# Optimization experiments

Measured on AMD Instinct MI355X. Metric: run time of the kernel, lower is better.

Reference implementation:

```python
import jax, jax.numpy as jnp
import numpy as np
from jax import lax

B, C_IN, C_OUT, H, W, K, PAD = 4, 64, 64, 96, 96, 3, 1
K2 = K * K


def setup_inputs() -> dict:
    key = jax.random.key(0)
    k1, k2, k3, k4, k5 = jax.random.split(key, 5)
    x = jax.random.normal(k1, (B, C_IN, H, W), jnp.float32)
    offset = jax.random.normal(k2, (B, 2 * K2, H, W), jnp.float32)
    weight = jax.random.normal(k3, (C_OUT, C_IN, K, K), jnp.float32) * 0.05
    mask_weight = jax.random.normal(k4, (K2, C_IN, K, K), jnp.float32) * 0.05
    mask_bias = jax.random.normal(k5, (K2,), jnp.float32) * 0.05
    return {"x": x, "offset": offset, "weight": weight,
            "mask_weight": mask_weight, "mask_bias": mask_bias}


def _deform_conv2d(x, offset, weight, mask):
    # torchvision ordering: per kernel tap k, offset[:, 2k] is dy, offset[:, 2k+1] is dx
    off_y = offset[:, 0::2]  # [B, K2, H, W]
    off_x = offset[:, 1::2]
    ky, kx = jnp.meshgrid(jnp.arange(K), jnp.arange(K), indexing="ij")
    ky = ky.reshape(K2).astype(x.dtype)
    kx = kx.reshape(K2).astype(x.dtype)
    hh = jnp.arange(H, dtype=x.dtype)
    ww = jnp.arange(W, dtype=x.dtype)
    base_y = hh[None, :, None] - PAD + ky[:, None, None]   # [K2, H, 1]
    base_x = ww[None, None, :] - PAD + kx[:, None, None]   # [K2, 1, W]
    py = base_y[None] + off_y                               # [B, K2, H, W]
    px = base_x[None] + off_x

    y0 = jnp.floor(py)
    x0 = jnp.floor(px)
    wy = py - y0   # bilinear weights
    wx = px - x0
    y0i = y0.astype(jnp.int32)
    x0i = x0.astype(jnp.int32)

    x_flat = x.reshape(B, C_IN, H * W)

    def gather(yy, xx):
        valid = (yy >= 0) & (yy < H) & (xx >= 0) & (xx < W)
        idx = jnp.clip(yy, 0, H - 1) * W + jnp.clip(xx, 0, W - 1)  # [B,K2,H,W]
        idx_f = idx.reshape(B, -1)
        v = jax.vmap(lambda xf, i: xf[:, i])(x_flat, idx_f)  # [B, C, K2*H*W]
        v = v.reshape(B, C_IN, K2, H, W)
        return v * valid[:, None].astype(v.dtype)

    v00 = gather(y0i, x0i)
    v01 = gather(y0i, x0i + 1)
    v10 = gather(y0i + 1, x0i)
    v11 = gather(y0i + 1, x0i + 1)

    wy_ = wy[:, None]  # [B,1,K2,H,W]
    wx_ = wx[:, None]
    sampled = (v00 * (1 - wy_) * (1 - wx_) + v01 * (1 - wy_) * wx_
               + v10 * wy_ * (1 - wx_) + v11 * wy_ * wx_)
    sampled = sampled * mask[:, None]  # modulate by sigmoid mask

    w2 = weight.reshape(C_OUT, C_IN, K2)
    return jnp.einsum("bckhw,ock->bohw", sampled, w2)


def reference(x, offset, weight, mask_weight, mask_bias):
    mask_logits = lax.conv_general_dilated(
        x, mask_weight, window_strides=(1, 1), padding=[(PAD, PAD), (PAD, PAD)],
        dimension_numbers=("NCHW", "OIHW", "NCHW"))
    mask = jax.nn.sigmoid(mask_logits + mask_bias[None, :, None, None])
    return _deform_conv2d(x, offset, weight, mask)
```

## Files before the change

### kernel.cpp

```cpp
#include <hip/hip_runtime.h>
#include <math.h>

#define BB 4
#define CI 64
#define CO 64
#define HH 96
#define WW 96
#define HW (HH*WW)
#define K2 9
#define NT (HW/64)
#define PADC 1

typedef __attribute__((ext_vector_type(8))) short short8;
typedef __attribute__((ext_vector_type(4))) float float4v;

#define XT_USHORTS ((size_t)BB*HW*64)
#define WF_USHORTS (18*64*32)
#define MWF_USHORTS (18*16*32)

__device__ __forceinline__ float bf2f(short s) {
    return __uint_as_float(((unsigned int)(unsigned short)s) << 16);
}
__device__ __forceinline__ short f2bf(float f) {
    unsigned int u = __float_as_uint(f);
    u = (u + 0x7fffu + ((u >> 16) & 1u)) >> 16;
    return (short)u;
}

__device__ __forceinline__ void unswz(int bid, int* b, int* tile) {
    int g = bid & 7, r = bid >> 3;
    *b = g & 3;
    *tile = (g >> 2) * 72 + r;
}

__global__ __launch_bounds__(256) void xt_kernel(const float* __restrict__ x,
                                                 unsigned short* __restrict__ xT) {
    __shared__ unsigned short ts[64][72];
    int t = threadIdx.x;
    int b, tl; unswz(blockIdx.x, &b, &tl);
    int p0 = tl * 64;
    const float* xb = x + (size_t)b * CI * HW + p0;
    int pq = t & 15, cg = t >> 4;
    #pragma unroll
    for (int i = 0; i < 4; i++) {
        int c = cg + i * 16;
        float4v v = *(const float4v*)(xb + (size_t)c * HW + pq * 4);
        ts[pq * 4 + 0][c] = (unsigned short)f2bf(v[0]);
        ts[pq * 4 + 1][c] = (unsigned short)f2bf(v[1]);
        ts[pq * 4 + 2][c] = (unsigned short)f2bf(v[2]);
        ts[pq * 4 + 3][c] = (unsigned short)f2bf(v[3]);
    }
    __syncthreads();
    int px = t >> 2, cq = t & 3;
    unsigned short* xo = xT + ((size_t)b * HW + p0 + px) * 64 + cq * 16;
    short8 v0 = *(const short8*)&ts[px][cq * 16];
    short8 v1 = *(const short8*)&ts[px][cq * 16 + 8];
    *(short8*)xo = v0;
    *(short8*)(xo + 8) = v1;
}

__global__ __launch_bounds__(256) void pack_kernel(const float* __restrict__ wgt,
                                                   const float* __restrict__ mw,
                                                   unsigned short* __restrict__ Wf,
                                                   unsigned short* __restrict__ MWf) {
    int i = blockIdx.x * 256 + threadIdx.x;
    if (i < WF_USHORTS) {
        int frag = i >> 11;
        int o = (i >> 5) & 63;
        int tt = i & 31;
        int k = frag >> 1, cc = frag & 1;
        int c = cc * 32 + tt;
        Wf[i] = (unsigned short)f2bf(wgt[o * 576 + c * 9 + k]);
    } else if (i < WF_USHORTS + MWF_USHORTS) {
        int e = i - WF_USHORTS;
        int frag = e >> 9;
        int m = (e >> 5) & 15;
        int tt = e & 31;
        int q = frag >> 1, cc = frag & 1;
        int c = cc * 32 + tt;
        MWf[e] = (m < 9) ? (unsigned short)f2bf(mw[m * 576 + c * 9 + q]) : 0;
    }
}

__global__ __launch_bounds__(256) void fused_kernel(const float* __restrict__ off,
                                                    const float* __restrict__ mbias,
                                                    const unsigned short* __restrict__ xT,
                                                    const unsigned short* __restrict__ Wf,
                                                    const unsigned short* __restrict__ MWf,
                                                    float* __restrict__ out) {
    __shared__ float s_mask[K2][64];
    __shared__ int   s_idx[K2][4][64];
    __shared__ float s_w[K2][4][64];

    int t = threadIdx.x;
    int lane = t & 63, wv = t >> 6;
    int n = lane & 15, quad = lane >> 4;
    int b, tl; unswz(blockIdx.x, &b, &tl);
    int p0 = tl * 64;
    int pxl = wv * 16 + n;
    int p = p0 + pxl;
    int h = p / WW, wc = p % WW;
    const unsigned short* xTb = xT + (size_t)b * HW * 64;

    {
        float4v acc = {0.f, 0.f, 0.f, 0.f};
        #pragma unroll
        for (int q = 0; q < 9; q++) {
            int hh = h + q / 3 - 1, ww2 = wc + q % 3 - 1;
            bool valid = (hh >= 0) && (hh < HH) && (ww2 >= 0) && (ww2 < WW);
            int nidx = valid ? (hh * WW + ww2) : 0;
            const unsigned short* src = xTb + (size_t)nidx * 64 + quad * 8;
            #pragma unroll
            for (int cc = 0; cc < 2; cc++) {
                short8 bfrag = {0, 0, 0, 0, 0, 0, 0, 0};
                if (valid) bfrag = *(const short8*)(src + cc * 32);
                short8 afrag = *(const short8*)(MWf + ((size_t)((q * 2 + cc) * 16 + n)) * 32 + quad * 8);
                acc = __builtin_amdgcn_mfma_f32_16x16x32_bf16(afrag, bfrag, acc, 0, 0, 0);
            }
        }
        #pragma unroll
        for (int r = 0; r < 4; r++) {
            int row = quad * 4 + r;
            if (row < 9) {
                float s = acc[r] + mbias[row];
                s_mask[row][pxl] = 1.f / (1.f + expf(-s));
            }
        }
    }
    __syncthreads();

    for (int e = t; e < K2 * 64; e += 256) {
        int k = e >> 6, pe = e & 63;
        int pp = p0 + pe;
        int hh0 = pp / WW, ww0 = pp % WW;
        int ky = k / 3, kx = k % 3;
        float oy = off[((size_t)b * 2 * K2 + 2 * k) * HW + pp];
        float ox = off[((size_t)b * 2 * K2 + 2 * k + 1) * HW + pp];
        float m = s_mask[k][pe];
        float py = (float)(hh0 - PADC + ky) + oy;
        float pxf = (float)(ww0 - PADC + kx) + ox;
        float y0f = floorf(py), x0f = floorf(pxf);
        float wy = py - y0f, wx = pxf - x0f;
        int y0 = (int)y0f, x0 = (int)x0f;
        int y1 = y0 + 1, x1 = x0 + 1;
        int y0c = min(max(y0, 0), HH - 1), y1c = min(max(y1, 0), HH - 1);
        int x0c = min(max(x0, 0), WW - 1), x1c = min(max(x1, 0), WW - 1);
        bool vy0 = (y0 >= 0) && (y0 < HH), vy1 = (y1 >= 0) && (y1 < HH);
        bool vx0 = (x0 >= 0) && (x0 < WW), vx1 = (x1 >= 0) && (x1 < WW);
        float w00 = (1.f - wy) * (1.f - wx) * m; if (!(vy0 && vx0)) w00 = 0.f;
        float w01 = (1.f - wy) * wx * m;         if (!(vy0 && vx1)) w01 = 0.f;
        float w10 = wy * (1.f - wx) * m;         if (!(vy1 && vx0)) w10 = 0.f;
        float w11 = wy * wx * m;                 if (!(vy1 && vx1)) w11 = 0.f;
        s_idx[k][0][pe] = y0c * WW + x0c;
        s_idx[k][1][pe] = y0c * WW + x1c;
        s_idx[k][2][pe] = y1c * WW + x0c;
        s_idx[k][3][pe] = y1c * WW + x1c;
        s_w[k][0][pe] = w00; s_w[k][1][pe] = w01;
        s_w[k][2][pe] = w10; s_w[k][3][pe] = w11;
    }
    __syncthreads();

    float4v acc0 = {0.f, 0.f, 0.f, 0.f};
    float4v acc1 = {0.f, 0.f, 0.f, 0.f};
    float4v acc2 = {0.f, 0.f, 0.f, 0.f};
    float4v acc3 = {0.f, 0.f, 0.f, 0.f};

    const unsigned short* xq = xTb + quad * 8;
    short8 st[2][8];

    auto loadK = [&](int k, short8* dst) {
        int i0 = s_idx[k][0][pxl], i1 = s_idx[k][1][pxl];
        int i2 = s_idx[k][2][pxl], i3 = s_idx[k][3][pxl];
        dst[0] = *(const short8*)(xq + (size_t)i0 * 64);
        dst[1] = *(const short8*)(xq + (size_t)i0 * 64 + 32);
        dst[2] = *(const short8*)(xq + (size_t)i1 * 64);
        dst[3] = *(const short8*)(xq + (size_t)i1 * 64 + 32);
        dst[4] = *(const short8*)(xq + (size_t)i2 * 64);
        dst[5] = *(const short8*)(xq + (size_t)i2 * 64 + 32);
        dst[6] = *(const short8*)(xq + (size_t)i3 * 64);
        dst[7] = *(const short8*)(xq + (size_t)i3 * 64 + 32);
    };

    loadK(0, st[0]);
    loadK(1, st[1]);

    #pragma unroll
    for (int k = 0; k < 9; k++) {
        float w0 = s_w[k][0][pxl], w1 = s_w[k][1][pxl];
        float w2 = s_w[k][2][pxl], w3 = s_w[k][3][pxl];
        short8 cur[8];
        #pragma unroll
        for (int j = 0; j < 8; j++) cur[j] = st[k & 1][j];
        if (k + 2 < 9) loadK(k + 2, st[k & 1]);
        #pragma unroll
        for (int cc = 0; cc < 2; cc++) {
            short8 bfrag;
            #pragma unroll
            for (int j = 0; j < 8; j++) {
                float v = bf2f(cur[cc][j])     * w0 + bf2f(cur[2 + cc][j]) * w1 +
                          bf2f(cur[4 + cc][j]) * w2 + bf2f(cur[6 + cc][j]) * w3;
                bfrag[j] = f2bf(v);
            }
            const unsigned short* wp = Wf + (size_t)((k * 2 + cc) * 64) * 32 + quad * 8;
            short8 a0 = *(const short8*)(wp + (0 * 16 + n) * 32);
            short8 a1 = *(const short8*)(wp + (1 * 16 + n) * 32);
            short8 a2 = *(const short8*)(wp + (2 * 16 + n) * 32);
            short8 a3 = *(const short8*)(wp + (3 * 16 + n) * 32);
            acc0 = __builtin_amdgcn_mfma_f32_16x16x32_bf16(a0, bfrag, acc0, 0, 0, 0);
            acc1 = __builtin_amdgcn_mfma_f32_16x16x32_bf16(a1, bfrag, acc1, 0, 0, 0);
            acc2 = __builtin_amdgcn_mfma_f32_16x16x32_bf16(a2, bfrag, acc2, 0, 0, 0);
            acc3 = __builtin_amdgcn_mfma_f32_16x16x32_bf16(a3, bfrag, acc3, 0, 0, 0);
        }
    }

    float* ob = out + (size_t)b * CO * HW + p0 + pxl;
    #pragma unroll
    for (int r = 0; r < 4; r++) {
        ob[(size_t)(0 * 16 + quad * 4 + r) * HW] = acc0[r];
        ob[(size_t)(1 * 16 + quad * 4 + r) * HW] = acc1[r];
        ob[(size_t)(2 * 16 + quad * 4 + r) * HW] = acc2[r];
        ob[(size_t)(3 * 16 + quad * 4 + r) * HW] = acc3[r];
    }
}

extern "C" void kernel_launch(void* const* d_in, const int* in_sizes, int n_in,
                              void* d_out, int out_size, void* d_ws, size_t ws_size,
                              hipStream_t stream) {
    const float* x   = (const float*)d_in[0];
    const float* off = (const float*)d_in[1];
    const float* wgt = (const float*)d_in[2];
    const float* mw  = (const float*)d_in[3];
    const float* mb  = (const float*)d_in[4];
    float* out = (float*)d_out;

    unsigned short* xT  = (unsigned short*)d_ws;
    unsigned short* Wf  = xT + XT_USHORTS;
    unsigned short* MWf = Wf + WF_USHORTS;

    hipLaunchKernelGGL(xt_kernel, dim3(BB * NT), dim3(256), 0, stream, x, xT);
    hipLaunchKernelGGL(pack_kernel, dim3((WF_USHORTS + MWF_USHORTS + 255) / 256), dim3(256),
                       0, stream, wgt, mw, Wf, MWf);
    hipLaunchKernelGGL(fused_kernel, dim3(BB * NT), dim3(256), 0, stream,
                       off, mb, xT, Wf, MWf, out);
}
```

Baseline: 122.2 us.

## Split input channels across waves with half-size pixel tiles and merge prep kernels

The fused kernel now handles 32 pixels per block and splits the 64 input channels between pairs of waves. Mask logits and output partial sums are reduced through shared memory, and the grid doubles, which raises parallelism and cuts per-thread gather and register load. The transpose and weight-pack kernels are merged into one launch to save launch overhead. In exchange it adds an extra barrier and LDS reduction, and it drops the two-stage software prefetch of gathered values.

```diff
diff --git a/kernel.cpp b/kernel.cpp
--- a/kernel.cpp
+++ b/kernel.cpp
@@ -9,6 +9,8 @@
 #define HW (HH*WW)
 #define K2 9
 #define NT (HW/64)
+#define TPX 32
+#define NTT (HW/TPX)
 #define PADC 1
 
 typedef __attribute__((ext_vector_type(8))) short short8;
@@ -27,58 +29,62 @@
     return (short)u;
 }
 
-__device__ __forceinline__ void unswz(int bid, int* b, int* tile) {
+__device__ __forceinline__ void unswz64(int bid, int* b, int* tile) {
     int g = bid & 7, r = bid >> 3;
     *b = g & 3;
     *tile = (g >> 2) * 72 + r;
 }
-
-__global__ __launch_bounds__(256) void xt_kernel(const float* __restrict__ x,
-                                                 unsigned short* __restrict__ xT) {
+__device__ __forceinline__ void unswz32(int bid, int* b, int* tile) {
+    int g = bid & 7, r = bid >> 3;
+    *b = g & 3;
+    *tile = (g >> 2) * 144 + r;
+}
+
+__global__ __launch_bounds__(256) void prep_kernel(const float* __restrict__ x,
+                                                   const float* __restrict__ wgt,
+                                                   const float* __restrict__ mw,
+                                                   unsigned short* __restrict__ xT,
+                                                   unsigned short* __restrict__ Wf,
+                                                   unsigned short* __restrict__ MWf) {
     __shared__ unsigned short ts[64][72];
     int t = threadIdx.x;
-    int b, tl; unswz(blockIdx.x, &b, &tl);
-    int p0 = tl * 64;
-    const float* xb = x + (size_t)b * CI * HW + p0;
-    int pq = t & 15, cg = t >> 4;
-    #pragma unroll
-    for (int i = 0; i < 4; i++) {
-        int c = cg + i * 16;
-        float4v v = *(const float4v*)(xb + (size_t)c * HW + pq * 4);
-        ts[pq * 4 + 0][c] = (unsigned short)f2bf(v[0]);
-        ts[pq * 4 + 1][c] = (unsigned short)f2bf(v[1]);
-        ts[pq * 4 + 2][c] = (unsigned short)f2bf(v[2]);
-        ts[pq * 4 + 3][c] = (unsigned short)f2bf(v[3]);
-    }
-    __syncthreads();
-    int px = t >> 2, cq = t & 3;
-    unsigned short* xo = xT + ((size_t)b * HW + p0 + px) * 64 + cq * 16;
-    short8 v0 = *(const short8*)&ts[px][cq * 16];
-    short8 v1 = *(const short8*)&ts[px][cq * 16 + 8];
-    *(short8*)xo = v0;
-    *(short8*)(xo + 8) = v1;
-}
-
-__global__ __launch_bounds__(256) void pack_kernel(const float* __restrict__ wgt,
-                                                   const float* __restrict__ mw,
-                                                   unsigned short* __restrict__ Wf,
-                                                   unsigned short* __restrict__ MWf) {
-    int i = blockIdx.x * 256 + threadIdx.x;
-    if (i < WF_USHORTS) {
-        int frag = i >> 11;
-        int o = (i >> 5) & 63;
-        int tt = i & 31;
-        int k = frag >> 1, cc = frag & 1;
-        int c = cc * 32 + tt;
-        Wf[i] = (unsigned short)f2bf(wgt[o * 576 + c * 9 + k]);
-    } else if (i < WF_USHORTS + MWF_USHORTS) {
-        int e = i - WF_USHORTS;
-        int frag = e >> 9;
-        int m = (e >> 5) & 15;
-        int tt = e & 31;
-        int q = frag >> 1, cc = frag & 1;
-        int c = cc * 32 + tt;
-        MWf[e] = (m < 9) ? (unsigned short)f2bf(mw[m * 576 + c * 9 + q]) : 0;
+    if (blockIdx.x < BB * NT) {
+        int b, tl; unswz64(blockIdx.x, &b, &tl);
+        int p0 = tl * 64;
+        const float* xb = x + (size_t)b * CI * HW + p0;
+        int pq = t & 15, cg = t >> 4;
+        #pragma unroll
+        for (int i = 0; i < 4; i++) {
+            int c = cg + i * 16;
+            float4v v = *(const float4v*)(xb + (size_t)c * HW + pq * 4);
+            ts[pq * 4 + 0][c] = (unsigned short)f2bf(v[0]);
+            ts[pq * 4 + 1][c] = (unsigned short)f2bf(v[1]);
+            ts[pq * 4 + 2][c] = (unsigned short)f2bf(v[2]);
+            ts[pq * 4 + 3][c] = (unsigned short)f2bf(v[3]);
+        }
+        __syncthreads();
+        int px = t >> 2, cq = t & 3;
+        unsigned short* xo = xT + ((size_t)b * HW + p0 + px) * 64 + cq * 16;
+        *(short8*)xo       = *(const short8*)&ts[px][cq * 16];
+        *(short8*)(xo + 8) = *(const short8*)&ts[px][cq * 16 + 8];
+    } else {
+        int i = (blockIdx.x - BB * NT) * 256 + t;
+        if (i < WF_USHORTS) {
+            int frag = i >> 11;
+            int o = (i >> 5) & 63;
+            int tt = i & 31;
+            int k = frag >> 1, cc = frag & 1;
+            int c = cc * 32 + tt;
+            Wf[i] = (unsigned short)f2bf(wgt[o * 576 + c * 9 + k]);
+        } else if (i < WF_USHORTS + MWF_USHORTS) {
+            int e = i - WF_USHORTS;
+            int frag = e >> 9;
+            int m = (e >> 5) & 15;
+            int tt = e & 31;
+            int q = frag >> 1, cc = frag & 1;
+            int c = cc * 32 + tt;
+            MWf[e] = (m < 9) ? (unsigned short)f2bf(mw[m * 576 + c * 9 + q]) : 0;
+        }
     }
 }
 
@@ -88,55 +94,52 @@
                                                     const unsigned short* __restrict__ Wf,
                                                     const unsigned short* __restrict__ MWf,
                                                     float* __restrict__ out) {
-    __shared__ float s_mask[K2][64];
-    __shared__ int   s_idx[K2][4][64];
-    __shared__ float s_w[K2][4][64];
+    __shared__ float s_mred[2][K2][TPX];
+    __shared__ int   s_idx[K2][4][TPX];
+    __shared__ float s_w[K2][4][TPX];
+    __shared__ float s_part[2][16][64];
 
     int t = threadIdx.x;
     int lane = t & 63, wv = t >> 6;
+    int pg = wv & 1, ch = wv >> 1;
     int n = lane & 15, quad = lane >> 4;
-    int b, tl; unswz(blockIdx.x, &b, &tl);
-    int p0 = tl * 64;
-    int pxl = wv * 16 + n;
+    int b, tl; unswz32(blockIdx.x, &b, &tl);
+    int p0 = tl * TPX;
+    int pxl = pg * 16 + n;
     int p = p0 + pxl;
     int h = p / WW, wc = p % WW;
     const unsigned short* xTb = xT + (size_t)b * HW * 64;
+    int cbase = ch * 32 + quad * 8;
 
     {
-        float4v acc = {0.f, 0.f, 0.f, 0.f};
+        float4v macc = {0.f, 0.f, 0.f, 0.f};
         #pragma unroll
         for (int q = 0; q < 9; q++) {
             int hh = h + q / 3 - 1, ww2 = wc + q % 3 - 1;
             bool valid = (hh >= 0) && (hh < HH) && (ww2 >= 0) && (ww2 < WW);
             int nidx = valid ? (hh * WW + ww2) : 0;
-            const unsigned short* src = xTb + (size_t)nidx * 64 + quad * 8;
-            #pragma unroll
-            for (int cc = 0; cc < 2; cc++) {
-                short8 bfrag = {0, 0, 0, 0, 0, 0, 0, 0};
-                if (valid) bfrag = *(const short8*)(src + cc * 32);
-                short8 afrag = *(const short8*)(MWf + ((size_t)((q * 2 + cc) * 16 + n)) * 32 + quad * 8);
-                acc = __builtin_amdgcn_mfma_f32_16x16x32_bf16(afrag, bfrag, acc, 0, 0, 0);
-            }
+            short8 bfrag = {0, 0, 0, 0, 0, 0, 0, 0};
+            if (valid) bfrag = *(const short8*)(xTb + (size_t)nidx * 64 + cbase);
+            short8 afrag = *(const short8*)(MWf + ((size_t)((q * 2 + ch) * 16 + n)) * 32 + quad * 8);
+            macc = __builtin_amdgcn_mfma_f32_16x16x32_bf16(afrag, bfrag, macc, 0, 0, 0);
         }
         #pragma unroll
         for (int r = 0; r < 4; r++) {
             int row = quad * 4 + r;
-            if (row < 9) {
-                float s = acc[r] + mbias[row];
-                s_mask[row][pxl] = 1.f / (1.f + expf(-s));
-            }
+            if (row < 9) s_mred[ch][row][pxl] = macc[r];
         }
     }
     __syncthreads();
 
-    for (int e = t; e < K2 * 64; e += 256) {
-        int k = e >> 6, pe = e & 63;
+    for (int e = t; e < K2 * TPX; e += 256) {
+        int k = e >> 5, pe = e & 31;
         int pp = p0 + pe;
         int hh0 = pp / WW, ww0 = pp % WW;
         int ky = k / 3, kx = k % 3;
         float oy = off[((size_t)b * 2 * K2 + 2 * k) * HW + pp];
         float ox = off[((size_t)b * 2 * K2 + 2 * k + 1) * HW + pp];
-        float m = s_mask[k][pe];
+        float s = s_mred[0][k][pe] + s_mred[1][k][pe] + mbias[k];
+        float m = 1.f / (1.f + expf(-s));
         float py = (float)(hh0 - PADC + ky) + oy;
         float pxf = (float)(ww0 - PADC + kx) + ox;
         float y0f = floorf(py), x0f = floorf(pxf);
@@ -164,62 +167,55 @@
     float4v acc1 = {0.f, 0.f, 0.f, 0.f};
     float4v acc2 = {0.f, 0.f, 0.f, 0.f};
     float4v acc3 = {0.f, 0.f, 0.f, 0.f};
-
-    const unsigned short* xq = xTb + quad * 8;
-    short8 st[2][8];
-
-    auto loadK = [&](int k, short8* dst) {
+    const unsigned short* xq = xTb + cbase;
+
+    #pragma unroll
+    for (int k = 0; k < 9; k++) {
         int i0 = s_idx[k][0][pxl], i1 = s_idx[k][1][pxl];
         int i2 = s_idx[k][2][pxl], i3 = s_idx[k][3][pxl];
-        dst[0] = *(const short8*)(xq + (size_t)i0 * 64);
-        dst[1] = *(const short8*)(xq + (size_t)i0 * 64 + 32);
-        dst[2] = *(const short8*)(xq + (size_t)i1 * 64);
-        dst[3] = *(const short8*)(xq + (size_t)i1 * 64 + 32);
-        dst[4] = *(const short8*)(xq + (size_t)i2 * 64);
-        dst[5] = *(const short8*)(xq + (size_t)i2 * 64 + 32);
-        dst[6] = *(const short8*)(xq + (size_t)i3 * 64);
-        dst[7] = *(const short8*)(xq + (size_t)i3 * 64 + 32);
-    };
-
-    loadK(0, st[0]);
-    loadK(1, st[1]);
-
-    #pragma unroll
-    for (int k = 0; k < 9; k++) {
         float w0 = s_w[k][0][pxl], w1 = s_w[k][1][pxl];
         float w2 = s_w[k][2][pxl], w3 = s_w[k][3][pxl];
-        short8 cur[8];
-        #pragma unroll
-        for (int j = 0; j < 8; j++) cur[j] = st[k & 1][j];
-        if (k + 2 < 9) loadK(k + 2, st[k & 1]);
-        #pragma unroll
-        for (int cc = 0; cc < 2; cc++) {
-            short8 bfrag;
-            #pragma unroll
-            for (int j = 0; j < 8; j++) {
-                float v = bf2f(cur[cc][j])     * w0 + bf2f(cur[2 + cc][j]) * w1 +
-                          bf2f(cur[4 + cc][j]) * w2 + bf2f(cur[6 + cc][j]) * w3;
-                bfrag[j] = f2bf(v);
-            }
-            const unsigned short* wp = Wf + (size_t)((k * 2 + cc) * 64) * 32 + quad * 8;
-            short8 a0 = *(const short8*)(wp + (0 * 16 + n) * 32);
-            short8 a1 = *(const short8*)(wp + (1 * 16 + n) * 32);
-            short8 a2 = *(const short8*)(wp + (2 * 16 + n) * 32);
-            short8 a3 = *(const short8*)(wp + (3 * 16 + n) * 32);
-            acc0 = __builtin_amdgcn_mfma_f32_16x16x32_bf16(a0, bfrag, acc0, 0, 0, 0);
-            acc1 = __builtin_amdgcn_mfma_f32_16x16x32_bf16(a1, bfrag, acc1, 0, 0, 0);
-            acc2 = __builtin_amdgcn_mfma_f32_16x16x32_bf16(a2, bfrag, acc2, 0, 0, 0);
-            acc3 = __builtin_amdgcn_mfma_f32_16x16x32_bf16(a3, bfrag, acc3, 0, 0, 0);
-        }
-    }
-
-    float* ob = out + (size_t)b * CO * HW + p0 + pxl;
-    #pragma unroll
-    for (int r = 0; r < 4; r++) {
-        ob[(size_t)(0 * 16 + quad * 4 + r) * HW] = acc0[r];
-        ob[(size_t)(1 * 16 + quad * 4 + r) * HW] = acc1[r];
-        ob[(size_t)(2 * 16 + quad * 4 + r) * HW] = acc2[r];
-        ob[(size_t)(3 * 16 + quad * 4 + r) * HW] = acc3[r];
+        short8 u0 = *(const short8*)(xq + (size_t)i0 * 64);
+        short8 u1 = *(const short8*)(xq + (size_t)i1 * 64);
+        short8 u2 = *(const short8*)(xq + (size_t)i2 * 64);
+        short8 u3 = *(const short8*)(xq + (size_t)i3 * 64);
+        short8 bfrag;
+        #pragma unroll
+        for (int j = 0; j < 8; j++) {
+            float v = bf2f(u0[j]) * w0 + bf2f(u1[j]) * w1 +
+                      bf2f(u2[j]) * w2 + bf2f(u3[j]) * w3;
+            bfrag[j] = f2bf(v);
+        }
+        const unsigned short* wp = Wf + (size_t)((k * 2 + ch) * 64) * 32 + quad * 8;
+        short8 a0 = *(const short8*)(wp + (0 * 16 + n) * 32);
+        short8 a1 = *(const short8*)(wp + (1 * 16 + n) * 32);
+        short8 a2 = *(const short8*)(wp + (2 * 16 + n) * 32);
+        short8 a3 = *(const short8*)(wp + (3 * 16 + n) * 32);
+        acc0 = __builtin_amdgcn_mfma_f32_16x16x32_bf16(a0, bfrag, acc0, 0, 0, 0);
+        acc1 = __builtin_amdgcn_mfma_f32_16x16x32_bf16(a1, bfrag, acc1, 0, 0, 0);
+        acc2 = __builtin_amdgcn_mfma_f32_16x16x32_bf16(a2, bfrag, acc2, 0, 0, 0);
+        acc3 = __builtin_amdgcn_mfma_f32_16x16x32_bf16(a3, bfrag, acc3, 0, 0, 0);
+    }
+
+    if (ch == 1) {
+        #pragma unroll
+        for (int r = 0; r < 4; r++) {
+            s_part[pg][0 * 4 + r][lane] = acc0[r];
+            s_part[pg][1 * 4 + r][lane] = acc1[r];
+            s_part[pg][2 * 4 + r][lane] = acc2[r];
+            s_part[pg][3 * 4 + r][lane] = acc3[r];
+        }
+    }
+    __syncthreads();
+    if (ch == 0) {
+        float* ob = out + (size_t)b * CO * HW + p0 + pxl;
+        #pragma unroll
+        for (int r = 0; r < 4; r++) {
+            ob[(size_t)(0 * 16 + quad * 4 + r) * HW] = acc0[r] + s_part[pg][0 * 4 + r][lane];
+            ob[(size_t)(1 * 16 + quad * 4 + r) * HW] = acc1[r] + s_part[pg][1 * 4 + r][lane];
+            ob[(size_t)(2 * 16 + quad * 4 + r) * HW] = acc2[r] + s_part[pg][2 * 4 + r][lane];
+            ob[(size_t)(3 * 16 + quad * 4 + r) * HW] = acc3[r] + s_part[pg][3 * 4 + r][lane];
+        }
     }
 }
 
@@ -237,9 +233,9 @@
     unsigned short* Wf  = xT + XT_USHORTS;
     unsigned short* MWf = Wf + WF_USHORTS;
 
-    hipLaunchKernelGGL(xt_kernel, dim3(BB * NT), dim3(256), 0, stream, x, xT);
-    hipLaunchKernelGGL(pack_kernel, dim3((WF_USHORTS + MWF_USHORTS + 255) / 256), dim3(256),
-                       0, stream, wgt, mw, Wf, MWf);
-    hipLaunchKernelGGL(fused_kernel, dim3(BB * NT), dim3(256), 0, stream,
+    int prep_grid = BB * NT + (WF_USHORTS + MWF_USHORTS + 255) / 256;
+    hipLaunchKernelGGL(prep_kernel, dim3(prep_grid), dim3(256), 0, stream,
+                       x, wgt, mw, xT, Wf, MWf);
+    hipLaunchKernelGGL(fused_kernel, dim3(BB * NTT), dim3(256), 0, stream,
                        off, mb, xT, Wf, MWf, out);
 }
```

After: 112.1 us. 1.09x faster.
